# Kernel optimization log

Hardware: AMD Instinct MI355X
Metric: run time of the kernel (lower is better)

Reference implementation:

```python
import jax, jax.numpy as jnp
import numpy as np

N, E, G = 100000, 400000, 4096
IN_F, H, D = 27, 4, 32
OUT_DIM = 128
EPS = 1e-5


def setup_inputs() -> dict:
    key = jax.random.key(0)
    ks = jax.random.split(key, 16)
    nrm = lambda k, s, sc=0.1: jax.random.normal(k, s, dtype=jnp.float32) * sc
    return dict(
        node_feats=nrm(ks[0], (N, IN_F), 1.0),
        src=jax.random.randint(ks[1], (E,), 0, N, dtype=jnp.int32),
        dst=jax.random.randint(ks[2], (E,), 0, N, dtype=jnp.int32),
        graph_ids=jnp.sort(jax.random.randint(ks[3], (N,), 0, G, dtype=jnp.int32)),
        # GAT layer 1 (27 -> 4 heads x 32, flatten + ELU, residual fc)
        fc1_w=nrm(ks[4], (H * D, IN_F)),
        attn_l1=nrm(ks[5], (H, D)), attn_r1=nrm(ks[6], (H, D)),
        res1_w=nrm(ks[7], (H * D, IN_F)), bias1=nrm(ks[8], (H, D)),
        # GAT layer 2 (128 -> 4 heads x 32, mean over heads, identity residual)
        fc2_w=nrm(ks[9], (H * D, H * D)),
        attn_l2=nrm(ks[10], (H, D)), attn_r2=nrm(ks[11], (H, D)),
        bias2=nrm(ks[12], (H, D)),
        # WeightedSumAndMax atom weighting
        aw_w=nrm(ks[13], (1, D)), aw_b=jnp.zeros((1,), jnp.float32),
        # gnn_last: Linear(2*32 -> 128)
        out_w=nrm(ks[14], (OUT_DIM, 2 * D)), out_b=jnp.zeros((OUT_DIM,), jnp.float32),
    )


def _gat_conv(h, src, dst, fc_w, a_l, a_r, bias, resval):
    # h: (N, F_in); returns (N, H, D)
    feat = (h @ fc_w.T).reshape(-1, H, D)            # (N, H, D)
    el = jnp.sum(feat * a_l, axis=-1)                # (N, H)
    er = jnp.sum(feat * a_r, axis=-1)                # (N, H)
    e = jax.nn.leaky_relu(el[src] + er[dst], 0.2)    # (E, H)
    # edge softmax over incoming edges of each dst node
    m = jax.ops.segment_max(e, dst, num_segments=N)
    ex = jnp.exp(e - m[dst])
    s = jax.ops.segment_sum(ex, dst, num_segments=N)
    a = ex / s[dst]                                  # (E, H)
    rst = jax.ops.segment_sum(feat[src] * a[..., None], dst, num_segments=N)
    return rst + resval + bias


def reference(node_feats, src, dst, graph_ids,
              fc1_w, attn_l1, attn_r1, res1_w, bias1,
              fc2_w, attn_l2, attn_r2, bias2,
              aw_w, aw_b, out_w, out_b):
    # --- GAT layer 1: flatten heads + ELU, residual via res_fc ---
    res1 = (node_feats @ res1_w.T).reshape(-1, H, D)
    h = _gat_conv(node_feats, src, dst, fc1_w, attn_l1, attn_r1, bias1, res1)
    h = jax.nn.elu(h.reshape(-1, H * D))             # (N, 128)
    # --- GAT layer 2: mean over heads, identity residual (in == H*D) ---
    res2 = h.reshape(-1, H, D)
    h = _gat_conv(h, src, dst, fc2_w, attn_l2, attn_r2, bias2, res2)
    h = jnp.mean(h, axis=1)                          # (N, 32)
    # --- WeightedSumAndMax readout ---
    w = jax.nn.sigmoid(h @ aw_w.T + aw_b)            # (N, 1)
    sum_g = jax.ops.segment_sum(w * h, graph_ids, num_segments=G)
    max_g = jax.ops.segment_max(h, graph_ids, num_segments=G)
    max_g = jnp.where(jnp.isfinite(max_g), max_g, 0.0)  # empty graphs -> 0
    g = jnp.concatenate([sum_g, max_g], axis=-1)     # (G, 64)
    # --- gnn_last + LayerNorm (no affine) ---
    y = g @ out_w.T + out_b                          # (G, 128)
    mu = jnp.mean(y, axis=-1, keepdims=True)
    var = jnp.mean(jnp.square(y - mu), axis=-1, keepdims=True)
    return (y - mu) / jnp.sqrt(var + EPS)
```

## Files before the change

### kernel.cpp

```cpp
#include <hip/hip_runtime.h>
#include <math.h>

#define NN 100000
#define EE 400000
#define GG 4096
#define INF_ 27
#define CC 128
#define HH 4
#define DD 32
#define NB 98

typedef short bf16x8 __attribute__((ext_vector_type(8)));
typedef float f32x4 __attribute__((ext_vector_type(4)));

static __device__ __forceinline__ unsigned short f2bf(float f){
  unsigned u = __float_as_uint(f);
  u += 0x7fffu + ((u>>16)&1u);
  return (unsigned short)(u>>16);
}
static __device__ __forceinline__ float bf2f(unsigned short s){
  return __uint_as_float(((unsigned)s)<<16);
}

__global__ void k_init0(int* __restrict__ deg){
  int i = blockIdx.x*blockDim.x + threadIdx.x;
  if (i < NN) deg[i]=0;
}

__global__ void k_count(const int* __restrict__ dst, int* __restrict__ deg){
  int i = blockIdx.x*blockDim.x + threadIdx.x;
  if (i < EE) atomicAdd(&deg[dst[i]], 1);
}

__global__ __launch_bounds__(256) void k_scan_local(const int* __restrict__ deg,
                                                    int* __restrict__ rowptr,
                                                    int* __restrict__ bsum){
  __shared__ int sh[256];
  int t = threadIdx.x;
  int idx = blockIdx.x*1024 + t*4;
  int v0 = (idx+0<NN)?deg[idx+0]:0;
  int v1 = (idx+1<NN)?deg[idx+1]:0;
  int v2 = (idx+2<NN)?deg[idx+2]:0;
  int v3 = (idx+3<NN)?deg[idx+3]:0;
  sh[t] = v0+v1+v2+v3;
  __syncthreads();
  for (int o=1;o<256;o<<=1){
    int x = (t>=o)? sh[t-o] : 0;
    __syncthreads();
    sh[t] += x;
    __syncthreads();
  }
  int run = (t==0)? 0 : sh[t-1];
  if (t==255) bsum[blockIdx.x] = sh[255];
  if (idx+0<NN){ rowptr[idx+0]=run; run+=v0; }
  if (idx+1<NN){ rowptr[idx+1]=run; run+=v1; }
  if (idx+2<NN){ rowptr[idx+2]=run; run+=v2; }
  if (idx+3<NN){ rowptr[idx+3]=run; }
}

__global__ void k_scan_bsums(int* __restrict__ bsum, int* __restrict__ rowptr){
  if (threadIdx.x==0 && blockIdx.x==0){
    int run = 0;
    for (int b=0;b<NB;b++){ int v=bsum[b]; bsum[b]=run; run+=v; }
    rowptr[NN] = run;
  }
}

__global__ __launch_bounds__(256) void k_scan_add(int* __restrict__ rowptr,
                                                  const int* __restrict__ bsum,
                                                  int* __restrict__ cursor){
  int idx = blockIdx.x*1024 + threadIdx.x*4;
  int off = bsum[blockIdx.x];
  #pragma unroll
  for (int i=0;i<4;i++){
    if (idx+i<NN){ int r = rowptr[idx+i]+off; rowptr[idx+i]=r; cursor[idx+i]=r; }
  }
}

__global__ void k_scatter(const int* __restrict__ src, const int* __restrict__ dst,
                          int* __restrict__ cursor, int* __restrict__ csr_src){
  int i = blockIdx.x*blockDim.x + threadIdx.x;
  if (i < EE){
    int pos = atomicAdd(&cursor[dst[i]], 1);
    csr_src[pos] = src[i];
  }
}

__global__ void k_graph_ptr(const int* __restrict__ gid, int* __restrict__ gptr){
  int i = blockIdx.x*blockDim.x + threadIdx.x;
  if (i >= NN) return;
  int g = gid[i];
  int gp = (i==0) ? -1 : gid[i-1];
  for (int q=gp+1; q<=g; q++) gptr[q] = i;
  if (i==NN-1){
    for (int q=g+1; q<=GG; q++) gptr[q] = NN;
  }
}

__global__ void k_cvtw2(const float* __restrict__ w, unsigned short* __restrict__ wb){
  int i = blockIdx.x*256 + threadIdx.x;
  if (i < CC*CC) wb[i] = f2bf(w[i]);
}

__global__ __launch_bounds__(128) void k_feat1(
    const float* __restrict__ x, const float* __restrict__ fcw,
    const float* __restrict__ resw, const float* __restrict__ bias,
    const float* __restrict__ al, const float* __restrict__ ar,
    unsigned short* __restrict__ featb, unsigned short* __restrict__ resb,
    float* __restrict__ el, float* __restrict__ er)
{
  __shared__ float xs[8*INF_];
  const int t = threadIdx.x;
  float w1r[INF_], w2r[INF_];
  #pragma unroll
  for (int k=0;k<INF_;k++){ w1r[k]=fcw[t*INF_+k]; w2r[k]=resw[t*INF_+k]; }
  const float alv = al[t], arv = ar[t], bv = bias[t];
  for (int base = blockIdx.x*8; base < NN; base += gridDim.x*8){
    __syncthreads();
    int nb = min(8, NN-base);
    int cnt = nb*INF_;
    for (int i=t;i<cnt;i+=128) xs[i] = x[base*INF_ + i];
    __syncthreads();
    for (int i=0;i<nb;i++){
      int n = base+i;
      float vf=0.f, vr=0.f;
      #pragma unroll
      for (int k=0;k<INF_;k++){
        float xv = xs[i*INF_+k];
        vf = fmaf(xv, w1r[k], vf);
        vr = fmaf(xv, w2r[k], vr);
      }
      featb[(size_t)n*CC+t] = f2bf(vf);
      resb[(size_t)n*CC+t]  = f2bf(vr + bv);
      float la = vf*alv, ra = vf*arv;
      #pragma unroll
      for (int o=16;o;o>>=1){ la += __shfl_xor(la,o,32); ra += __shfl_xor(ra,o,32); }
      if ((t&31)==0){ el[n*HH+(t>>5)] = la; er[n*HH+(t>>5)] = ra; }
    }
  }
}

__global__ __launch_bounds__(256) void k_feat2(
    const unsigned short* __restrict__ hb, const unsigned short* __restrict__ wb2,
    const float* __restrict__ al, const float* __restrict__ ar,
    unsigned short* __restrict__ featb, float* __restrict__ el, float* __restrict__ er)
{
  int wid = (blockIdx.x*256 + threadIdx.x) >> 6;
  int lane = threadIdx.x & 63;
  int tile = wid >> 1;
  int ch = wid & 1;
  if (tile >= NN/16) return;
  int l15 = lane & 15, khi = lane >> 4;
  int n0 = tile*16;
  bf16x8 wf[4][4];
  #pragma unroll
  for (int ct=0; ct<4; ct++)
    #pragma unroll
    for (int ks=0; ks<4; ks++)
      wf[ct][ks] = *(const bf16x8*)(wb2 + (size_t)(ch*64+ct*16+l15)*CC + ks*32 + khi*8);
  bf16x8 af[4];
  #pragma unroll
  for (int ks=0; ks<4; ks++)
    af[ks] = *(const bf16x8*)(hb + (size_t)(n0+l15)*CC + ks*32 + khi*8);
  f32x4 accf[4] = {{0.f,0.f,0.f,0.f},{0.f,0.f,0.f,0.f},{0.f,0.f,0.f,0.f},{0.f,0.f,0.f,0.f}};
  #pragma unroll
  for (int ks=0; ks<4; ks++)
    #pragma unroll
    for (int ct=0; ct<4; ct++)
      accf[ct] = __builtin_amdgcn_mfma_f32_16x16x32_bf16(af[ks], wf[ct][ks], accf[ct], 0,0,0);
  #pragma unroll
  for (int ct=0; ct<4; ct++)
    #pragma unroll
    for (int r=0;r<4;r++)
      featb[(size_t)(n0+khi*4+r)*CC + ch*64+ct*16+l15] = f2bf(accf[ct][r]);
  #pragma unroll
  for (int hh=0; hh<2; hh++){
    int c0 = ch*64 + hh*32 + l15;
    float a0 = al[c0], a1 = al[c0+16], b0 = ar[c0], b1 = ar[c0+16];
    #pragma unroll
    for (int r=0;r<4;r++){
      float pe = accf[2*hh][r]*a0 + accf[2*hh+1][r]*a1;
      float pr = accf[2*hh][r]*b0 + accf[2*hh+1][r]*b1;
      #pragma unroll
      for (int o=8;o;o>>=1){ pe += __shfl_xor(pe,o,16); pr += __shfl_xor(pr,o,16); }
      if (l15==0){
        int n = n0 + khi*4 + r;
        el[n*HH + ch*2+hh] = pe;
        er[n*HH + ch*2+hh] = pr;
      }
    }
  }
}

__global__ __launch_bounds__(256) void k_aggr1(
    const int* __restrict__ rowptr, const int* __restrict__ csr,
    const float* __restrict__ el, const float* __restrict__ er,
    const unsigned short* __restrict__ featb,
    const unsigned short* __restrict__ resb,
    unsigned short* __restrict__ hb)
{
  int t = threadIdx.x;
  int n = blockIdx.x*8 + (t>>5);
  if (n >= NN) return;
  int lane = t & 31;
  int h = lane >> 3;
  int e0 = rowptr[n], e1 = rowptr[n+1];
  float ern = er[n*HH + h];
  float ssum = 0.f;
  float r0=0.f,r1=0.f,r2=0.f,r3=0.f;
  int j = e0;
  for (; j+2 <= e1; j += 2){
    int sa = csr[j], sb = csr[j+1];
    float va = el[sa*HH+h] + ern; va = va>0.f?va:0.2f*va;
    float vb = el[sb*HH+h] + ern; vb = vb>0.f?vb:0.2f*vb;
    float aa = __expf(va), ab = __expf(vb);
    ssum += aa + ab;
    ushort4 fa = *(const ushort4*)(featb + (size_t)sa*CC + lane*4);
    ushort4 fb = *(const ushort4*)(featb + (size_t)sb*CC + lane*4);
    r0 = fmaf(bf2f(fa.x), aa, r0); r1 = fmaf(bf2f(fa.y), aa, r1);
    r2 = fmaf(bf2f(fa.z), aa, r2); r3 = fmaf(bf2f(fa.w), aa, r3);
    r0 = fmaf(bf2f(fb.x), ab, r0); r1 = fmaf(bf2f(fb.y), ab, r1);
    r2 = fmaf(bf2f(fb.z), ab, r2); r3 = fmaf(bf2f(fb.w), ab, r3);
  }
  if (j < e1){
    int sa = csr[j];
    float va = el[sa*HH+h] + ern; va = va>0.f?va:0.2f*va;
    float aa = __expf(va);
    ssum += aa;
    ushort4 fa = *(const ushort4*)(featb + (size_t)sa*CC + lane*4);
    r0 = fmaf(bf2f(fa.x), aa, r0); r1 = fmaf(bf2f(fa.y), aa, r1);
    r2 = fmaf(bf2f(fa.z), aa, r2); r3 = fmaf(bf2f(fa.w), aa, r3);
  }
  float inv = (e1 > e0) ? 1.f/ssum : 0.f;
  ushort4 rv = *(const ushort4*)(resb + (size_t)n*CC + lane*4);
  float t0 = bf2f(rv.x) + r0*inv;
  float t1 = bf2f(rv.y) + r1*inv;
  float t2 = bf2f(rv.z) + r2*inv;
  float t3 = bf2f(rv.w) + r3*inv;
  t0 = t0 > 0.f ? t0 : __expf(t0)-1.f;
  t1 = t1 > 0.f ? t1 : __expf(t1)-1.f;
  t2 = t2 > 0.f ? t2 : __expf(t2)-1.f;
  t3 = t3 > 0.f ? t3 : __expf(t3)-1.f;
  ushort4 hb4; hb4.x=f2bf(t0); hb4.y=f2bf(t1); hb4.z=f2bf(t2); hb4.w=f2bf(t3);
  *(ushort4*)(hb + (size_t)n*CC + lane*4) = hb4;
}

__global__ __launch_bounds__(256) void k_aggr2(
    const int* __restrict__ gptr, const int* __restrict__ rowptr,
    const int* __restrict__ csr,
    const float* __restrict__ el, const float* __restrict__ er,
    const unsigned short* __restrict__ featb,
    const unsigned short* __restrict__ hb,
    const float* __restrict__ b2, const float* __restrict__ aww,
    const float* __restrict__ awb,
    const float* __restrict__ outw, const float* __restrict__ outb,
    float* __restrict__ out)
{
  __shared__ float lsum[8][32];
  __shared__ float lmax[8][32];
  __shared__ float gv[64];
  __shared__ float rr1[2], rr2[2];
  int g = blockIdx.x;
  int n0 = gptr[g], n1 = gptr[g+1];
  int t = threadIdx.x;
  int grp = t>>5, lane = t&31, h = lane>>3;
  float gs0=0.f,gs1=0.f,gs2=0.f,gs3=0.f;
  float gm0=-3.4e38f,gm1=-3.4e38f,gm2=-3.4e38f,gm3=-3.4e38f;
  float4 bv  = *(const float4*)(b2 + lane*4);
  float4 aw4 = *(const float4*)(aww + (lane&7)*4);
  float awbv = awb[0];
  for (int n = n0+grp; n < n1; n += 8){
    int e0 = rowptr[n], e1 = rowptr[n+1];
    float ern = er[n*HH + h];
    float ssum = 0.f;
    float r0=0.f,r1=0.f,r2=0.f,r3=0.f;
    int j = e0;
    for (; j+2 <= e1; j += 2){
      int sa = csr[j], sb = csr[j+1];
      float va = el[sa*HH+h] + ern; va = va>0.f?va:0.2f*va;
      float vb = el[sb*HH+h] + ern; vb = vb>0.f?vb:0.2f*vb;
      float aa = __expf(va), ab = __expf(vb);
      ssum += aa + ab;
      ushort4 fa = *(const ushort4*)(featb + (size_t)sa*CC + lane*4);
      ushort4 fb = *(const ushort4*)(featb + (size_t)sb*CC + lane*4);
      r0 = fmaf(bf2f(fa.x), aa, r0); r1 = fmaf(bf2f(fa.y), aa, r1);
      r2 = fmaf(bf2f(fa.z), aa, r2); r3 = fmaf(bf2f(fa.w), aa, r3);
      r0 = fmaf(bf2f(fb.x), ab, r0); r1 = fmaf(bf2f(fb.y), ab, r1);
      r2 = fmaf(bf2f(fb.z), ab, r2); r3 = fmaf(bf2f(fb.w), ab, r3);
    }
    if (j < e1){
      int sa = csr[j];
      float va = el[sa*HH+h] + ern; va = va>0.f?va:0.2f*va;
      float aa = __expf(va);
      ssum += aa;
      ushort4 fa = *(const ushort4*)(featb + (size_t)sa*CC + lane*4);
      r0 = fmaf(bf2f(fa.x), aa, r0); r1 = fmaf(bf2f(fa.y), aa, r1);
      r2 = fmaf(bf2f(fa.z), aa, r2); r3 = fmaf(bf2f(fa.w), aa, r3);
    }
    float inv = (e1 > e0) ? 1.f/ssum : 0.f;
    ushort4 hv = *(const ushort4*)(hb + (size_t)n*CC + lane*4);
    float t0 = bf2f(hv.x) + bv.x + r0*inv;
    float t1 = bf2f(hv.y) + bv.y + r1*inv;
    float t2 = bf2f(hv.z) + bv.z + r2*inv;
    float t3 = bf2f(hv.w) + bv.w + r3*inv;
    float s0=t0,s1=t1,s2=t2,s3=t3;
    s0 += __shfl_xor(s0,8,32);  s1 += __shfl_xor(s1,8,32);
    s2 += __shfl_xor(s2,8,32);  s3 += __shfl_xor(s3,8,32);
    s0 += __shfl_xor(s0,16,32); s1 += __shfl_xor(s1,16,32);
    s2 += __shfl_xor(s2,16,32); s3 += __shfl_xor(s3,16,32);
    float hm0=0.25f*s0, hm1=0.25f*s1, hm2=0.25f*s2, hm3=0.25f*s3;
    float p = hm0*aw4.x + hm1*aw4.y + hm2*aw4.z + hm3*aw4.w;
    p += __shfl_xor(p,1,32); p += __shfl_xor(p,2,32); p += __shfl_xor(p,4,32);
    float wgt = 1.f/(1.f + __expf(-(p + awbv)));
    gs0 = fmaf(wgt, hm0, gs0); gs1 = fmaf(wgt, hm1, gs1);
    gs2 = fmaf(wgt, hm2, gs2); gs3 = fmaf(wgt, hm3, gs3);
    gm0 = fmaxf(gm0, hm0); gm1 = fmaxf(gm1, hm1);
    gm2 = fmaxf(gm2, hm2); gm3 = fmaxf(gm3, hm3);
  }
  if (lane < 8){
    int c = lane*4;
    lsum[grp][c+0]=gs0; lsum[grp][c+1]=gs1; lsum[grp][c+2]=gs2; lsum[grp][c+3]=gs3;
    lmax[grp][c+0]=gm0; lmax[grp][c+1]=gm1; lmax[grp][c+2]=gm2; lmax[grp][c+3]=gm3;
  }
  __syncthreads();
  if (t < 32){
    float s=0.f, m=-3.4e38f;
    #pragma unroll
    for (int q=0;q<8;q++){ s += lsum[q][t]; m = fmaxf(m, lmax[q][t]); }
    gv[t]    = s;
    gv[32+t] = (m < -3.0e38f) ? 0.f : m;
  }
  __syncthreads();
  float y = 0.f;
  if (t < 128){
    y = outb[t];
    #pragma unroll
    for (int jj=0;jj<64;jj++) y = fmaf(gv[jj], outw[t*64+jj], y);
    float s1 = y, s2 = y*y;
    #pragma unroll
    for (int o=32;o;o>>=1){ s1 += __shfl_xor(s1,o); s2 += __shfl_xor(s2,o); }
    if ((t&63)==0){ rr1[t>>6]=s1; rr2[t>>6]=s2; }
  }
  __syncthreads();
  if (t < 128){
    float S1 = rr1[0]+rr1[1], S2 = rr2[0]+rr2[1];
    float mu = S1*(1.f/128.f);
    float var = S2*(1.f/128.f) - mu*mu;
    out[g*CC + t] = (y - mu) * rsqrtf(var + 1e-5f);
  }
}

extern "C" void kernel_launch(void* const* d_in, const int* in_sizes, int n_in,
                              void* d_out, int out_size, void* d_ws, size_t ws_size,
                              hipStream_t stream){
  const float* x     = (const float*)d_in[0];
  const int*   src   = (const int*)d_in[1];
  const int*   dst   = (const int*)d_in[2];
  const int*   gid   = (const int*)d_in[3];
  const float* fc1w  = (const float*)d_in[4];
  const float* al1   = (const float*)d_in[5];
  const float* ar1   = (const float*)d_in[6];
  const float* res1w = (const float*)d_in[7];
  const float* b1    = (const float*)d_in[8];
  const float* fc2w  = (const float*)d_in[9];
  const float* al2   = (const float*)d_in[10];
  const float* ar2   = (const float*)d_in[11];
  const float* b2    = (const float*)d_in[12];
  const float* aww   = (const float*)d_in[13];
  const float* awb   = (const float*)d_in[14];
  const float* outw  = (const float*)d_in[15];
  const float* outb  = (const float*)d_in[16];
  float* out = (float*)d_out;

  char* w = (char*)d_ws;
  unsigned short* featb = (unsigned short*)w;  w += (size_t)NN*CC*2;
  unsigned short* hb    = (unsigned short*)w;  w += (size_t)NN*CC*2;
  unsigned short* resb  = (unsigned short*)w;  w += (size_t)NN*CC*2;
  float*          el    = (float*)w;           w += (size_t)NN*HH*4;
  float*          er    = (float*)w;           w += (size_t)NN*HH*4;
  int*            deg   = (int*)w;             w += (size_t)NN*4;
  int*            rowptr= (int*)w;             w += (size_t)(NN+1)*4;
  int*            cursor= (int*)w;             w += (size_t)NN*4;
  int*            bsum  = (int*)w;             w += 128*4;
  int*            csr   = (int*)w;             w += (size_t)EE*4;
  int*            gptr  = (int*)w;             w += (size_t)(GG+1)*4;
  unsigned short* wb2   = (unsigned short*)w;  w += (size_t)CC*CC*2;

  const int EB = (EE + 255)/256;
  const int NBK = (NN + 255)/256;

  k_init0<<<NBK,256,0,stream>>>(deg);
  k_count<<<EB,256,0,stream>>>(dst, deg);
  k_scan_local<<<NB,256,0,stream>>>(deg, rowptr, bsum);
  k_scan_bsums<<<1,64,0,stream>>>(bsum, rowptr);
  k_scan_add<<<NB,256,0,stream>>>(rowptr, bsum, cursor);
  k_scatter<<<EB,256,0,stream>>>(src, dst, cursor, csr);
  k_graph_ptr<<<NBK,256,0,stream>>>(gid, gptr);
  k_cvtw2<<<(CC*CC+255)/256,256,0,stream>>>(fc2w, wb2);

  k_feat1<<<1250,128,0,stream>>>(x, fc1w, res1w, b1, al1, ar1, featb, resb, el, er);
  k_aggr1<<<(NN+7)/8,256,0,stream>>>(rowptr, csr, el, er, featb, resb, hb);
  k_feat2<<<(NN/16*2+3)/4,256,0,stream>>>(hb, wb2, al2, ar2, featb, el, er);
  k_aggr2<<<GG,256,0,stream>>>(gptr, rowptr, csr, el, er, featb, hb,
                               b2, aww, awb, outw, outb, out);
}
```

Baseline: 237.5 us.

## Compute layer-1 projection and residual with bf16 MFMA on padded inputs

Replaces the scalar FMA layer-1 feature/residual projection with a bf16 MFMA 16x16x32 kernel, after converting node features and both weight matrices to zero-padded bf16 (K=32). Attention logits are now reduced across 16-lane groups from the MFMA accumulators. This moves the dense projection from vector ALUs to matrix cores. In exchange it adds two conversion kernels and an extra pass over x, and it rounds the inputs to bf16, which lowers precision. Output stores are scattered 2-byte writes per lane.

```diff
diff --git a/kernel.cpp b/kernel.cpp
--- a/kernel.cpp
+++ b/kernel.cpp
@@ -102,40 +102,81 @@
   if (i < CC*CC) wb[i] = f2bf(w[i]);
 }
 
-__global__ __launch_bounds__(128) void k_feat1(
-    const float* __restrict__ x, const float* __restrict__ fcw,
-    const float* __restrict__ resw, const float* __restrict__ bias,
+__global__ void k_cvtx(const float* __restrict__ x, unsigned short* __restrict__ xb){
+  int i = blockIdx.x*256 + threadIdx.x;
+  if (i >= NN*32) return;
+  int n = i>>5, k = i&31;
+  xb[i] = (k<INF_) ? f2bf(x[n*INF_+k]) : (unsigned short)0;
+}
+
+__global__ void k_cvtw1(const float* __restrict__ fcw, const float* __restrict__ resw,
+                        unsigned short* __restrict__ wb1, unsigned short* __restrict__ wrb){
+  int i = blockIdx.x*256 + threadIdx.x;
+  if (i >= CC*32) return;
+  int c = i>>5, k = i&31;
+  wb1[i] = (k<INF_) ? f2bf(fcw[c*INF_+k]) : (unsigned short)0;
+  wrb[i] = (k<INF_) ? f2bf(resw[c*INF_+k]) : (unsigned short)0;
+}
+
+__global__ __launch_bounds__(256) void k_feat1m(
+    const unsigned short* __restrict__ xb, const unsigned short* __restrict__ wb1,
+    const unsigned short* __restrict__ wrb, const float* __restrict__ bias,
     const float* __restrict__ al, const float* __restrict__ ar,
     unsigned short* __restrict__ featb, unsigned short* __restrict__ resb,
     float* __restrict__ el, float* __restrict__ er)
 {
-  __shared__ float xs[8*INF_];
-  const int t = threadIdx.x;
-  float w1r[INF_], w2r[INF_];
-  #pragma unroll
-  for (int k=0;k<INF_;k++){ w1r[k]=fcw[t*INF_+k]; w2r[k]=resw[t*INF_+k]; }
-  const float alv = al[t], arv = ar[t], bv = bias[t];
-  for (int base = blockIdx.x*8; base < NN; base += gridDim.x*8){
-    __syncthreads();
-    int nb = min(8, NN-base);
-    int cnt = nb*INF_;
-    for (int i=t;i<cnt;i+=128) xs[i] = x[base*INF_ + i];
-    __syncthreads();
-    for (int i=0;i<nb;i++){
-      int n = base+i;
-      float vf=0.f, vr=0.f;
+  int wid = (blockIdx.x*256 + threadIdx.x) >> 6;
+  int lane = threadIdx.x & 63;
+  int l15 = lane & 15, khi = lane >> 4;
+  int nw = gridDim.x*4;
+  bf16x8 wf[8], wr[8];
+  float bv8[8];
+  #pragma unroll
+  for (int ct=0; ct<8; ct++){
+    wf[ct] = *(const bf16x8*)(wb1 + (ct*16+l15)*32 + khi*8);
+    wr[ct] = *(const bf16x8*)(wrb + (ct*16+l15)*32 + khi*8);
+    bv8[ct] = bias[ct*16+l15];
+  }
+  float a0v[4], a1v[4], b0v[4], b1v[4];
+  #pragma unroll
+  for (int hh=0; hh<4; hh++){
+    int c0 = hh*32 + l15;
+    a0v[hh] = al[c0]; a1v[hh] = al[c0+16];
+    b0v[hh] = ar[c0]; b1v[hh] = ar[c0+16];
+  }
+  for (int tile = wid; tile < NN/16; tile += nw){
+    int n0 = tile*16;
+    bf16x8 af = *(const bf16x8*)(xb + (size_t)(n0+l15)*32 + khi*8);
+    f32x4 accf[8], accr[8];
+    #pragma unroll
+    for (int ct=0; ct<8; ct++){
+      accf[ct] = __builtin_amdgcn_mfma_f32_16x16x32_bf16(af, wf[ct], (f32x4){0.f,0.f,0.f,0.f}, 0,0,0);
+      accr[ct] = __builtin_amdgcn_mfma_f32_16x16x32_bf16(af, wr[ct], (f32x4){0.f,0.f,0.f,0.f}, 0,0,0);
+    }
+    #pragma unroll
+    for (int ct=0; ct<8; ct++){
+      int c = ct*16+l15;
       #pragma unroll
-      for (int k=0;k<INF_;k++){
-        float xv = xs[i*INF_+k];
-        vf = fmaf(xv, w1r[k], vf);
-        vr = fmaf(xv, w2r[k], vr);
+      for (int r=0;r<4;r++){
+        int n = n0 + khi*4 + r;
+        featb[(size_t)n*CC + c] = f2bf(accf[ct][r]);
+        resb [(size_t)n*CC + c] = f2bf(accr[ct][r] + bv8[ct]);
       }
-      featb[(size_t)n*CC+t] = f2bf(vf);
-      resb[(size_t)n*CC+t]  = f2bf(vr + bv);
-      float la = vf*alv, ra = vf*arv;
+    }
+    #pragma unroll
+    for (int hh=0; hh<4; hh++){
       #pragma unroll
-      for (int o=16;o;o>>=1){ la += __shfl_xor(la,o,32); ra += __shfl_xor(ra,o,32); }
-      if ((t&31)==0){ el[n*HH+(t>>5)] = la; er[n*HH+(t>>5)] = ra; }
+      for (int r=0;r<4;r++){
+        float pe = accf[2*hh][r]*a0v[hh] + accf[2*hh+1][r]*a1v[hh];
+        float pr = accf[2*hh][r]*b0v[hh] + accf[2*hh+1][r]*b1v[hh];
+        #pragma unroll
+        for (int o=8;o;o>>=1){ pe += __shfl_xor(pe,o,16); pr += __shfl_xor(pr,o,16); }
+        if (l15==0){
+          int n = n0 + khi*4 + r;
+          el[n*HH + hh] = pe;
+          er[n*HH + hh] = pr;
+        }
+      }
     }
   }
 }
@@ -385,6 +426,9 @@
   int*            csr   = (int*)w;             w += (size_t)EE*4;
   int*            gptr  = (int*)w;             w += (size_t)(GG+1)*4;
   unsigned short* wb2   = (unsigned short*)w;  w += (size_t)CC*CC*2;
+  unsigned short* xb    = (unsigned short*)w;  w += (size_t)NN*32*2;
+  unsigned short* wb1   = (unsigned short*)w;  w += (size_t)CC*32*2;
+  unsigned short* wrb   = (unsigned short*)w;  w += (size_t)CC*32*2;
 
   const int EB = (EE + 255)/256;
   const int NBK = (NN + 255)/256;
@@ -397,8 +441,10 @@
   k_scatter<<<EB,256,0,stream>>>(src, dst, cursor, csr);
   k_graph_ptr<<<NBK,256,0,stream>>>(gid, gptr);
   k_cvtw2<<<(CC*CC+255)/256,256,0,stream>>>(fc2w, wb2);
-
-  k_feat1<<<1250,128,0,stream>>>(x, fc1w, res1w, b1, al1, ar1, featb, resb, el, er);
+  k_cvtx<<<(NN*32+255)/256,256,0,stream>>>(x, xb);
+  k_cvtw1<<<(CC*32+255)/256,256,0,stream>>>(fc1w, res1w, wb1, wrb);
+
+  k_feat1m<<<1024,256,0,stream>>>(xb, wb1, wrb, b1, al1, ar1, featb, resb, el, er);
   k_aggr1<<<(NN+7)/8,256,0,stream>>>(rowptr, csr, el, er, featb, resb, hb);
   k_feat2<<<(NN/16*2+3)/4,256,0,stream>>>(hb, wb2, al2, ar2, featb, el, er);
   k_aggr2<<<GG,256,0,stream>>>(gptr, rowptr, csr, el, er, featb, hb,
```

Measured after the change: 215.2 us. 1.1x faster.
